# Kernel optimization log

Measured on AMD Instinct MI355X. Metric: run time of the kernel, lower is better.

Reference implementation:

```python
import jax, jax.numpy as jnp
import numpy as np

B, H, W, C, NC = 4, 64, 64, 64, 19


def setup_inputs() -> dict:
    key = jax.random.key(0)
    ks = jax.random.split(key, 12)
    s = 0.05  # small init so sigmoid scores are not saturated
    return {
        "feature": jax.random.normal(ks[0], (B, H, W, C), dtype=jnp.float32),
        "predict": jax.random.normal(ks[1], (B, H, W, NC), dtype=jnp.float32),
        # height attention params (dim = H); k_linear in source is unused (q reused as k)
        "hq_w": jax.random.normal(ks[2], (H, H), dtype=jnp.float32) * s,
        "hq_b": jnp.zeros((H,), dtype=jnp.float32),
        "hv_w": jax.random.normal(ks[3], (H, H), dtype=jnp.float32) * s,
        "hv_b": jnp.zeros((H,), dtype=jnp.float32),
        # width attention params (dim = W)
        "wq_w": jax.random.normal(ks[4], (W, W), dtype=jnp.float32) * s,
        "wq_b": jnp.zeros((W,), dtype=jnp.float32),
        "wv_w": jax.random.normal(ks[5], (W, W), dtype=jnp.float32) * s,
        "wv_b": jnp.zeros((W,), dtype=jnp.float32),
        # gating scalars (nn.Parameter(torch.zeros(1)) in source; random here to exercise path)
        "h_gate": jax.random.normal(ks[6], (1,), dtype=jnp.float32) * 0.5,
        "w_gate": jax.random.normal(ks[7], (1,), dtype=jnp.float32) * 0.5,
        # 1x1 conv num_classes -> 1 (stored as [NC, 1] matrix; 1x1 conv == per-pixel linear)
        "conv_w": jax.random.normal(ks[8], (NC, 1), dtype=jnp.float32) * s,
        "conv_b": jnp.zeros((1,), dtype=jnp.float32),
    }


def _self_atten(x, wq, bq, wv, bv, dim):
    # Source uses q_linear for BOTH q and k (k_linear dead), softmax replaced by sigmoid.
    q = x @ wq + bq                                   # [B, N, dim]
    v = x @ wv + bv                                   # [B, N, dim]
    scores = jax.nn.sigmoid(jnp.einsum('bnd,bmd->bnm', q, q) / jnp.sqrt(jnp.float32(dim)))
    return jnp.einsum('bnm,bmd->bnd', scores, v)      # [B, N, dim]


def _axial(x, hq_w, hq_b, hv_w, hv_b, wq_w, wq_b, wv_w, wv_b, h_gate, w_gate):
    b, h, w, c = x.shape
    # height attention: seq = W*C, feature dim = H
    xh = x.transpose(0, 2, 3, 1).reshape(b, w * c, h)
    xh = _self_atten(xh, hq_w, hq_b, hv_w, hv_b, h)
    xh = xh.reshape(b, w, c, h).transpose(0, 3, 1, 2)  # back to [B,H,W,C]
    x = xh * h_gate + x
    # width attention: seq = H*C, feature dim = W
    xw = x.transpose(0, 1, 3, 2).reshape(b, h * c, w)
    xw = _self_atten(xw, wq_w, wq_b, wv_w, wv_b, w)
    xw = xw.reshape(b, h, c, w).transpose(0, 1, 3, 2)  # back to [B,H,W,C]
    x = xw * w_gate + x
    return x


def reference(feature, predict, hq_w, hq_b, hv_w, hv_b, wq_w, wq_b, wv_w, wv_b,
              h_gate, w_gate, conv_w, conv_b):
    feat = feature + _axial(feature, hq_w, hq_b, hv_w, hv_b,
                            wq_w, wq_b, wv_w, wv_b, h_gate, w_gate)
    p = 1.0 - jax.nn.sigmoid(predict)                 # [B,H,W,NC]
    p = p @ conv_w + conv_b                           # 1x1 conv -> [B,H,W,1]
    return p * feat                                   # broadcast gate -> [B,H,W,C]
```

## Files before the change

kernel.cpp:

```cpp
#include <hip/hip_runtime.h>

typedef _Float16 f16x8 __attribute__((ext_vector_type(8)));
typedef __fp16   fp16x2 __attribute__((ext_vector_type(2)));
typedef float f32x16 __attribute__((ext_vector_type(16)));

__device__ __forceinline__ unsigned pkrtz(float a, float b) {
    fp16x2 h = __builtin_amdgcn_cvt_pkrtz(a, b);
    union { fp16x2 h; unsigned u; } c; c.h = h; return c.u;
}

__device__ __forceinline__ unsigned short f2h(float f) {
    _Float16 h = (_Float16)f;
    union { _Float16 h; unsigned short s; } c; c.h = h; return c.s;
}

__device__ __forceinline__ float sig_from_t(float t) {
    return __builtin_amdgcn_rcpf(1.0f + __builtin_exp2f(t));
}

__global__ __launch_bounds__(256) void prep_kernel(
    const float* __restrict__ src,
    const float* __restrict__ wq, const float* __restrict__ bq,
    const float* __restrict__ wv, const float* __restrict__ bv,
    unsigned short* __restrict__ Qg, unsigned short* __restrict__ Vtg)
{
    __shared__ float slab[64][65];
    __shared__ float wqs[4096];
    __shared__ float wvs[4096];

    const int t  = threadIdx.x;
    const int bx = blockIdx.x, b = blockIdx.y;

    {
        const float4* wq4 = (const float4*)wq;
        const float4* wv4 = (const float4*)wv;
        float4* q4 = (float4*)wqs; float4* v4 = (float4*)wvs;
        #pragma unroll
        for (int i = 0; i < 4; ++i) {
            q4[i*256 + t] = wq4[i*256 + t];
            v4[i*256 + t] = wv4[i*256 + t];
        }
    }
    {
        const int k = t >> 2, c0 = (t & 3) << 4;
        const size_t sb = (size_t)b*262144 + (size_t)k*4096 + (size_t)bx*64 + c0;
        #pragma unroll
        for (int i = 0; i < 4; ++i)
            *(float4*)&slab[k][c0 + i*4] = *(const float4*)&src[sb + i*4];
    }
    __syncthreads();

    const int c = t & 63, jg = t >> 6;
    float qa[16], va[16];
    #pragma unroll
    for (int jj = 0; jj < 16; ++jj) { qa[jj] = bq[jg*16+jj]; va[jj] = bv[jg*16+jj]; }
    for (int k = 0; k < 64; ++k) {
        const float xv = slab[k][c];
        const float* wqr = &wqs[k*64 + jg*16];
        const float* wvr = &wvs[k*64 + jg*16];
        #pragma unroll
        for (int jj = 0; jj < 16; ++jj) {
            qa[jj] += xv * wqr[jj];
            va[jj] += xv * wvr[jj];
        }
    }
    const int token = bx*64 + c;
    union { unsigned u[8]; uint4 v[2]; } qp;
    #pragma unroll
    for (int jj = 0; jj < 8; ++jj) qp.u[jj] = pkrtz(qa[2*jj], qa[2*jj+1]);
    const size_t qoff = ((size_t)b*4096 + token)*64 + jg*16;
    *(uint4*)&Qg[qoff]     = qp.v[0];
    *(uint4*)&Qg[qoff + 8] = qp.v[1];
    #pragma unroll
    for (int jj = 0; jj < 16; ++jj)
        Vtg[((size_t)b*64 + jg*16 + jj)*4096 + token] = f2h(va[jj]);
}

__global__ __launch_bounds__(256) void prep_w_kernel(
    const float* __restrict__ feature, const float* __restrict__ Pin,
    const float* __restrict__ gate,
    const float* __restrict__ wq, const float* __restrict__ bq,
    const float* __restrict__ wv, const float* __restrict__ bv,
    unsigned short* __restrict__ Qg, unsigned short* __restrict__ Vtg,
    float* __restrict__ x1out, int nsplit)
{
    __shared__ float slab[64][65];
    __shared__ float wqs[4096];
    __shared__ float wvs[4096];

    const int t  = threadIdx.x;
    const int bx = blockIdx.x, b = blockIdx.y;

    {
        const float4* wq4 = (const float4*)wq;
        const float4* wv4 = (const float4*)wv;
        float4* q4 = (float4*)wqs; float4* v4 = (float4*)wvs;
        #pragma unroll
        for (int i = 0; i < 4; ++i) {
            q4[i*256 + t] = wq4[i*256 + t];
            v4[i*256 + t] = wv4[i*256 + t];
        }
    }
    {
        const int k = t >> 2, c0 = (t & 3) << 4;
        const size_t off = (size_t)bx*4096 + (size_t)k*64 + c0;
        const size_t fb  = (size_t)b*262144 + off;
        const float g = gate[0];
        #pragma unroll
        for (int i = 0; i < 4; ++i) {
            float4 v  = *(const float4*)&feature[fb + i*4];
            float sx = 0.f, sy = 0.f, sz = 0.f, sw = 0.f;
            for (int ks = 0; ks < nsplit; ++ks) {
                float4 pk = *(const float4*)&Pin[((size_t)(ks*4 + b) << 18) + off + i*4];
                sx += pk.x; sy += pk.y; sz += pk.z; sw += pk.w;
            }
            v.x += g * sx; v.y += g * sy; v.z += g * sz; v.w += g * sw;
            *(float4*)&slab[k][c0 + i*4] = v;
            *(float4*)&x1out[fb + i*4] = v;
        }
    }
    __syncthreads();

    const int c = t & 63, jg = t >> 6;
    float qa[16], va[16];
    #pragma unroll
    for (int jj = 0; jj < 16; ++jj) { qa[jj] = bq[jg*16+jj]; va[jj] = bv[jg*16+jj]; }
    for (int k = 0; k < 64; ++k) {
        const float xv = slab[k][c];
        const float* wqr = &wqs[k*64 + jg*16];
        const float* wvr = &wvs[k*64 + jg*16];
        #pragma unroll
        for (int jj = 0; jj < 16; ++jj) {
            qa[jj] += xv * wqr[jj];
            va[jj] += xv * wvr[jj];
        }
    }
    const int token = bx*64 + c;
    union { unsigned u[8]; uint4 v[2]; } qp;
    #pragma unroll
    for (int jj = 0; jj < 8; ++jj) qp.u[jj] = pkrtz(qa[2*jj], qa[2*jj+1]);
    const size_t qoff = ((size_t)b*4096 + token)*64 + jg*16;
    *(uint4*)&Qg[qoff]     = qp.v[0];
    *(uint4*)&Qg[qoff + 8] = qp.v[1];
    #pragma unroll
    for (int jj = 0; jj < 16; ++jj)
        Vtg[((size_t)b*64 + jg*16 + jj)*4096 + token] = f2h(va[jj]);
}

__global__ __launch_bounds__(256) void attn_kernel(
    const unsigned short* __restrict__ Qg,
    const unsigned short* __restrict__ Vtg,
    float* __restrict__ P)
{
    __shared__ unsigned short Ksh[64][72];
    __shared__ unsigned short Vts[64][72];

    const int t = threadIdx.x;
    const int mb = blockIdx.x, b = blockIdx.y, ksplit = blockIdx.z;
    const int nsp = gridDim.z;
    const int niter = 64 / nsp;
    const int keybase = ksplit * (4096 / nsp);
    const int lane = t & 63, w = t >> 6;
    const int l32 = lane & 31, hi = lane >> 5;

    const unsigned short* Qbase = Qg  + (size_t)b*262144;
    const unsigned short* Vbase = Vtg + (size_t)b*262144;

    f16x8 qb[4];
    {
        const unsigned short* qrow = Qbase + (size_t)(mb*128 + w*32 + l32)*64 + hi*8;
        const _Float16 sc = (_Float16)(-0.180336880f);
        #pragma unroll
        for (int s = 0; s < 4; ++s) {
            f16x8 q = *(const f16x8*)(qrow + s*16);
            qb[s] = q * sc;
        }
    }

    f32x16 y[2];
    #pragma unroll
    for (int i = 0; i < 16; ++i) { y[0][i] = 0.f; y[1][i] = 0.f; }

    const int lrow = t >> 2;
    const int loff = (t & 3) << 4;
    {
        const uint4* gk = (const uint4*)(Qbase + (size_t)(keybase + lrow)*64 + loff);
        uint4 k0 = gk[0], k1 = gk[1];
        const uint4* gv = (const uint4*)(Vbase + (size_t)lrow*4096 + keybase + loff);
        uint4 v0 = gv[0], v1 = gv[1];
        *(uint4*)&Ksh[lrow][loff]     = k0;
        *(uint4*)&Ksh[lrow][loff + 8] = k1;
        *(uint4*)&Vts[lrow][loff]     = v0;
        *(uint4*)&Vts[lrow][loff + 8] = v1;
    }
    __syncthreads();

    for (int kb = 0; kb < niter; ++kb) {
        uint4 nk0 = {0,0,0,0}, nk1 = {0,0,0,0}, nv0 = {0,0,0,0}, nv1 = {0,0,0,0};
        if (kb < niter - 1) {
            const int keyn = keybase + (kb + 1)*64;
            const uint4* gk = (const uint4*)(Qbase + (size_t)(keyn + lrow)*64 + loff);
            nk0 = gk[0]; nk1 = gk[1];
            const uint4* gv = (const uint4*)(Vbase + (size_t)lrow*4096 + keyn + loff);
            nv0 = gv[0]; nv1 = gv[1];
        }

        f32x16 tt[2];
        #pragma unroll
        for (int i = 0; i < 16; ++i) { tt[0][i] = 0.f; tt[1][i] = 0.f; }
        #pragma unroll
        for (int s = 0; s < 4; ++s) {
            const int co = s*16 + hi*8;
            f16x8 ka0 = *(const f16x8*)&Ksh[l32][co];
            f16x8 ka1 = *(const f16x8*)&Ksh[32 + l32][co];
            tt[0] = __builtin_amdgcn_mfma_f32_32x32x16_f16(ka0, qb[s], tt[0], 0,0,0);
            tt[1] = __builtin_amdgcn_mfma_f32_32x32x16_f16(ka1, qb[s], tt[1], 0,0,0);
        }

        #pragma unroll
        for (int u = 0; u < 2; ++u) {
            float sg[16];
            #pragma unroll
            for (int r = 0; r < 16; ++r) sg[r] = sig_from_t(tt[u][r]);
            #pragma unroll
            for (int ksh = 0; ksh < 2; ++ksh) {
                const int bR = ksh*8;
                unsigned Pa = pkrtz(sg[bR+0], sg[bR+1]);
                unsigned Pb = pkrtz(sg[bR+2], sg[bR+3]);
                unsigned Qa = pkrtz(sg[bR+4], sg[bR+5]);
                unsigned Qb = pkrtz(sg[bR+6], sg[bR+7]);
                unsigned xPa = __shfl_xor(Pa, 32);
                unsigned xPb = __shfl_xor(Pb, 32);
                unsigned xQa = __shfl_xor(Qa, 32);
                unsigned xQb = __shfl_xor(Qb, 32);
                union { unsigned u[4]; f16x8 v; } sa;
                sa.u[0] = hi ? xQa : Pa;
                sa.u[1] = hi ? xQb : Pb;
                sa.u[2] = hi ? Qa : xPa;
                sa.u[3] = hi ? Qb : xPb;

                const int ks = u*2 + ksh;
                const int co = ks*16 + hi*8;
                f16x8 vb0 = *(const f16x8*)&Vts[l32][co];
                f16x8 vb1 = *(const f16x8*)&Vts[32 + l32][co];
                y[0] = __builtin_amdgcn_mfma_f32_32x32x16_f16(sa.v, vb0, y[0], 0,0,0);
                y[1] = __builtin_amdgcn_mfma_f32_32x32x16_f16(sa.v, vb1, y[1], 0,0,0);
            }
        }

        __syncthreads();
        if (kb < niter - 1) {
            *(uint4*)&Ksh[lrow][loff]     = nk0;
            *(uint4*)&Ksh[lrow][loff + 8] = nk1;
            *(uint4*)&Vts[lrow][loff]     = nv0;
            *(uint4*)&Vts[lrow][loff + 8] = nv1;
        }
        __syncthreads();
    }

    float* Pp = P + (((size_t)(ksplit*4 + b)) << 18);
    const int token0 = mb*128 + w*32 + hi*4;
    #pragma unroll
    for (int dt = 0; dt < 2; ++dt) {
        const int d = dt*32 + l32;
        #pragma unroll
        for (int g = 0; g < 4; ++g) {
            float4 v;
            v.x = y[dt][4*g+0]; v.y = y[dt][4*g+1];
            v.z = y[dt][4*g+2]; v.w = y[dt][4*g+3];
            *(float4*)&Pp[(size_t)d*4096 + token0 + 8*g] = v;
        }
    }
}

__global__ __launch_bounds__(256) void final_kernel(
    const float* __restrict__ feature, const float* __restrict__ x1,
    const float* __restrict__ Pin, const float* __restrict__ predict,
    const float* __restrict__ conv_w, const float* __restrict__ conv_b,
    const float* __restrict__ gate, float* __restrict__ out, int nsplit)
{
    const int i4 = blockIdx.x * 256 + threadIdx.x;
    const int j = i4 << 2;
    const int pix = j >> 6;
    const float* row = predict + (size_t)pix * 19;
    float pv = conv_b[0];
    #pragma unroll
    for (int i = 0; i < 19; ++i) {
        float sg = __builtin_amdgcn_rcpf(1.0f + __builtin_exp2f(-1.442695041f * row[i]));
        pv += (1.0f - sg) * conv_w[i];
    }

    const int b = j >> 18, h = (j >> 12) & 63, d = (j >> 6) & 63, c = j & 63;
    const size_t pif = ((size_t)(b*64 + d) << 12) + h*64 + c;
    float sx = 0.f, sy = 0.f, sz = 0.f, sw = 0.f;
    for (int ks = 0; ks < nsplit; ++ks) {
        float4 pk = *(const float4*)&Pin[((size_t)ks << 20) + pif];
        sx += pk.x; sy += pk.y; sz += pk.z; sw += pk.w;
    }
    const float g = gate[0];
    float4 f = ((const float4*)feature)[i4];
    float4 x = ((const float4*)x1)[i4];
    float4 o;
    o.x = pv * (f.x + x.x + g * sx);
    o.y = pv * (f.y + x.y + g * sy);
    o.z = pv * (f.z + x.z + g * sz);
    o.w = pv * (f.w + x.w + g * sw);
    ((float4*)out)[i4] = o;
}

extern "C" void kernel_launch(void* const* d_in, const int* in_sizes, int n_in,
                              void* d_out, int out_size, void* d_ws, size_t ws_size,
                              hipStream_t stream) {
    const float* feature = (const float*)d_in[0];
    const float* predict = (const float*)d_in[1];
    const float* hq_w = (const float*)d_in[2];
    const float* hq_b = (const float*)d_in[3];
    const float* hv_w = (const float*)d_in[4];
    const float* hv_b = (const float*)d_in[5];
    const float* wq_w = (const float*)d_in[6];
    const float* wq_b = (const float*)d_in[7];
    const float* wv_w = (const float*)d_in[8];
    const float* wv_b = (const float*)d_in[9];
    const float* h_gate = (const float*)d_in[10];
    const float* w_gate = (const float*)d_in[11];
    const float* conv_w = (const float*)d_in[12];
    const float* conv_b = (const float*)d_in[13];
    float* out = (float*)d_out;

    char* ws = (char*)d_ws;
    unsigned short* Qg  = (unsigned short*)(ws);
    unsigned short* Vtg = (unsigned short*)(ws + (2u << 20));
    float*          x1  = (float*)(ws + (4u << 20));
    float*          P   = (float*)(ws + (8u << 20));
    const int nsplit = 4;

    dim3 blk(256);
    prep_kernel<<<dim3(64, 4), blk, 0, stream>>>(feature, hq_w, hq_b, hv_w, hv_b,
                                                 Qg, Vtg);
    attn_kernel<<<dim3(32, 4, nsplit), blk, 0, stream>>>(Qg, Vtg, P);
    prep_w_kernel<<<dim3(64, 4), blk, 0, stream>>>(feature, P, h_gate,
                                                   wq_w, wq_b, wv_w, wv_b,
                                                   Qg, Vtg, x1, nsplit);
    attn_kernel<<<dim3(32, 4, nsplit), blk, 0, stream>>>(Qg, Vtg, P);
    final_kernel<<<dim3(1024), blk, 0, stream>>>(feature, x1, P, predict,
                                                 conv_w, conv_b, w_gate, out, nsplit);
}
```

Baseline: 189.2 us.

## Compute Q/V projections with fp16 MFMA using pre-transposed fp16 weights

Replaces the scalar FP32 LDS-based Q and V projection loops with 32x32x16 fp16 MFMA instructions. A new small kernel converts and transposes the four weight matrices to fp16 once per call. The two prep kernels are merged into one parameterized kernel with stride arguments, and the input tile is staged as fp16 in shared memory. This cuts per-block LDS weight loading and FMA work, but adds a launch, rounds inputs and weights to fp16, and switches to scalar uncoalesced stores for Q and the feature loads.

```diff
diff --git a/kernel.cpp b/kernel.cpp
--- a/kernel.cpp
+++ b/kernel.cpp
@@ -18,133 +18,108 @@
     return __builtin_amdgcn_rcpf(1.0f + __builtin_exp2f(t));
 }
 
+__global__ __launch_bounds__(256) void wprep_kernel(
+    const float* __restrict__ w0, const float* __restrict__ w1,
+    const float* __restrict__ w2, const float* __restrict__ w3,
+    unsigned short* __restrict__ Wt)
+{
+    __shared__ float m[64][65];
+    const float* src = (blockIdx.x == 0) ? w0 : (blockIdx.x == 1) ? w1
+                     : (blockIdx.x == 2) ? w2 : w3;
+    const int t = threadIdx.x;
+    const int k = t >> 2, c0 = (t & 3) << 4;
+    #pragma unroll
+    for (int i = 0; i < 4; ++i)
+        *(float4*)&m[k][c0 + i*4] = *(const float4*)&src[k*64 + c0 + i*4];
+    __syncthreads();
+    const int j = t >> 2, k0 = (t & 3) << 4;
+    union { unsigned u[8]; uint4 v[2]; } o;
+    #pragma unroll
+    for (int p = 0; p < 8; ++p) o.u[p] = pkrtz(m[k0 + 2*p][j], m[k0 + 2*p + 1][j]);
+    unsigned short* dst = Wt + blockIdx.x*4096 + j*64 + k0;
+    *(uint4*)dst       = o.v[0];
+    *(uint4*)(dst + 8) = o.v[1];
+}
+
 __global__ __launch_bounds__(256) void prep_kernel(
-    const float* __restrict__ src,
-    const float* __restrict__ wq, const float* __restrict__ bq,
-    const float* __restrict__ wv, const float* __restrict__ bv,
-    unsigned short* __restrict__ Qg, unsigned short* __restrict__ Vtg)
+    const float* __restrict__ src, const float* __restrict__ Pin,
+    const float* __restrict__ gate,
+    const unsigned short* __restrict__ Wqt, const unsigned short* __restrict__ Wvt,
+    const float* __restrict__ bq, const float* __restrict__ bv,
+    unsigned short* __restrict__ Qg, unsigned short* __restrict__ Vtg,
+    float* __restrict__ x1out, int sK, int sF, int nsplit)
 {
-    __shared__ float slab[64][65];
-    __shared__ float wqs[4096];
-    __shared__ float wvs[4096];
-
-    const int t  = threadIdx.x;
+    __shared__ unsigned short Xt[64][76];
+
+    const int t = threadIdx.x;
     const int bx = blockIdx.x, b = blockIdx.y;
 
     {
-        const float4* wq4 = (const float4*)wq;
-        const float4* wv4 = (const float4*)wv;
-        float4* q4 = (float4*)wqs; float4* v4 = (float4*)wvs;
-        #pragma unroll
-        for (int i = 0; i < 4; ++i) {
-            q4[i*256 + t] = wq4[i*256 + t];
-            v4[i*256 + t] = wv4[i*256 + t];
-        }
-    }
+        const int c = t & 63, kq = t >> 6;
+        const float g = Pin ? gate[0] : 0.f;
+        float vals[16];
+        #pragma unroll
+        for (int kk = 0; kk < 16; ++kk) {
+            const int k = kq*16 + kk;
+            const size_t off = (size_t)k*sK + (size_t)bx*sF + c;
+            float v = src[(size_t)b*262144 + off];
+            if (Pin) {
+                float s = 0.f;
+                for (int ks = 0; ks < nsplit; ++ks)
+                    s += Pin[((size_t)(ks*4 + b) << 18) + off];
+                v += g * s;
+                x1out[(size_t)b*262144 + off] = v;
+            }
+            vals[kk] = v;
+        }
+        union { unsigned u[8]; uint4 q[2]; } pk;
+        #pragma unroll
+        for (int p = 0; p < 8; ++p) pk.u[p] = pkrtz(vals[2*p], vals[2*p+1]);
+        *(uint4*)&Xt[c][kq*16]     = pk.q[0];
+        *(uint4*)&Xt[c][kq*16 + 8] = pk.q[1];
+    }
+    __syncthreads();
+
+    const int lane = t & 63, w = t >> 6;
+    const int l32 = lane & 31, hi = lane >> 5;
+    const int tt = w & 1, jt = w >> 1;
+
+    f16x8 xf[4], wqf[4], wvf[4];
+    #pragma unroll
+    for (int s = 0; s < 4; ++s)
+        xf[s] = *(const f16x8*)&Xt[tt*32 + l32][s*16 + hi*8];
     {
-        const int k = t >> 2, c0 = (t & 3) << 4;
-        const size_t sb = (size_t)b*262144 + (size_t)k*4096 + (size_t)bx*64 + c0;
-        #pragma unroll
-        for (int i = 0; i < 4; ++i)
-            *(float4*)&slab[k][c0 + i*4] = *(const float4*)&src[sb + i*4];
-    }
-    __syncthreads();
-
-    const int c = t & 63, jg = t >> 6;
-    float qa[16], va[16];
-    #pragma unroll
-    for (int jj = 0; jj < 16; ++jj) { qa[jj] = bq[jg*16+jj]; va[jj] = bv[jg*16+jj]; }
-    for (int k = 0; k < 64; ++k) {
-        const float xv = slab[k][c];
-        const float* wqr = &wqs[k*64 + jg*16];
-        const float* wvr = &wvs[k*64 + jg*16];
-        #pragma unroll
-        for (int jj = 0; jj < 16; ++jj) {
-            qa[jj] += xv * wqr[jj];
-            va[jj] += xv * wvr[jj];
-        }
-    }
-    const int token = bx*64 + c;
-    union { unsigned u[8]; uint4 v[2]; } qp;
-    #pragma unroll
-    for (int jj = 0; jj < 8; ++jj) qp.u[jj] = pkrtz(qa[2*jj], qa[2*jj+1]);
-    const size_t qoff = ((size_t)b*4096 + token)*64 + jg*16;
-    *(uint4*)&Qg[qoff]     = qp.v[0];
-    *(uint4*)&Qg[qoff + 8] = qp.v[1];
-    #pragma unroll
-    for (int jj = 0; jj < 16; ++jj)
-        Vtg[((size_t)b*64 + jg*16 + jj)*4096 + token] = f2h(va[jj]);
-}
-
-__global__ __launch_bounds__(256) void prep_w_kernel(
-    const float* __restrict__ feature, const float* __restrict__ Pin,
-    const float* __restrict__ gate,
-    const float* __restrict__ wq, const float* __restrict__ bq,
-    const float* __restrict__ wv, const float* __restrict__ bv,
-    unsigned short* __restrict__ Qg, unsigned short* __restrict__ Vtg,
-    float* __restrict__ x1out, int nsplit)
-{
-    __shared__ float slab[64][65];
-    __shared__ float wqs[4096];
-    __shared__ float wvs[4096];
-
-    const int t  = threadIdx.x;
-    const int bx = blockIdx.x, b = blockIdx.y;
-
-    {
-        const float4* wq4 = (const float4*)wq;
-        const float4* wv4 = (const float4*)wv;
-        float4* q4 = (float4*)wqs; float4* v4 = (float4*)wvs;
-        #pragma unroll
-        for (int i = 0; i < 4; ++i) {
-            q4[i*256 + t] = wq4[i*256 + t];
-            v4[i*256 + t] = wv4[i*256 + t];
-        }
-    }
-    {
-        const int k = t >> 2, c0 = (t & 3) << 4;
-        const size_t off = (size_t)bx*4096 + (size_t)k*64 + c0;
-        const size_t fb  = (size_t)b*262144 + off;
-        const float g = gate[0];
-        #pragma unroll
-        for (int i = 0; i < 4; ++i) {
-            float4 v  = *(const float4*)&feature[fb + i*4];
-            float sx = 0.f, sy = 0.f, sz = 0.f, sw = 0.f;
-            for (int ks = 0; ks < nsplit; ++ks) {
-                float4 pk = *(const float4*)&Pin[((size_t)(ks*4 + b) << 18) + off + i*4];
-                sx += pk.x; sy += pk.y; sz += pk.z; sw += pk.w;
-            }
-            v.x += g * sx; v.y += g * sy; v.z += g * sz; v.w += g * sw;
-            *(float4*)&slab[k][c0 + i*4] = v;
-            *(float4*)&x1out[fb + i*4] = v;
-        }
-    }
-    __syncthreads();
-
-    const int c = t & 63, jg = t >> 6;
-    float qa[16], va[16];
-    #pragma unroll
-    for (int jj = 0; jj < 16; ++jj) { qa[jj] = bq[jg*16+jj]; va[jj] = bv[jg*16+jj]; }
-    for (int k = 0; k < 64; ++k) {
-        const float xv = slab[k][c];
-        const float* wqr = &wqs[k*64 + jg*16];
-        const float* wvr = &wvs[k*64 + jg*16];
-        #pragma unroll
-        for (int jj = 0; jj < 16; ++jj) {
-            qa[jj] += xv * wqr[jj];
-            va[jj] += xv * wvr[jj];
-        }
-    }
-    const int token = bx*64 + c;
-    union { unsigned u[8]; uint4 v[2]; } qp;
-    #pragma unroll
-    for (int jj = 0; jj < 8; ++jj) qp.u[jj] = pkrtz(qa[2*jj], qa[2*jj+1]);
-    const size_t qoff = ((size_t)b*4096 + token)*64 + jg*16;
-    *(uint4*)&Qg[qoff]     = qp.v[0];
-    *(uint4*)&Qg[qoff + 8] = qp.v[1];
-    #pragma unroll
-    for (int jj = 0; jj < 16; ++jj)
-        Vtg[((size_t)b*64 + jg*16 + jj)*4096 + token] = f2h(va[jj]);
+        const unsigned short* qr = Wqt + (size_t)(jt*32 + l32)*64 + hi*8;
+        const unsigned short* vr = Wvt + (size_t)(jt*32 + l32)*64 + hi*8;
+        #pragma unroll
+        for (int s = 0; s < 4; ++s) {
+            wqf[s] = *(const f16x8*)(qr + s*16);
+            wvf[s] = *(const f16x8*)(vr + s*16);
+        }
+    }
+
+    f32x16 qa, va;
+    #pragma unroll
+    for (int i = 0; i < 16; ++i) { qa[i] = 0.f; va[i] = 0.f; }
+    #pragma unroll
+    for (int s = 0; s < 4; ++s) {
+        qa = __builtin_amdgcn_mfma_f32_32x32x16_f16(xf[s], wqf[s], qa, 0,0,0);
+        va = __builtin_amdgcn_mfma_f32_32x32x16_f16(wvf[s], xf[s], va, 0,0,0);
+    }
+
+    const float bqv = bq[jt*32 + l32];
+    const size_t qbase = (size_t)b*4096 + bx*64;
+    #pragma unroll
+    for (int r = 0; r < 16; ++r) {
+        const int c = tt*32 + (r & 3) + 8*(r >> 2) + 4*hi;
+        Qg[(qbase + c)*64 + jt*32 + l32] = f2h(qa[r] + bqv);
+    }
+    const int ctok = bx*64 + tt*32 + l32;
+    #pragma unroll
+    for (int r = 0; r < 16; ++r) {
+        const int j = jt*32 + (r & 3) + 8*(r >> 2) + 4*hi;
+        Vtg[(size_t)b*262144 + (size_t)j*4096 + ctok] = f2h(va[r] + bv[j]);
+    }
 }
 
 __global__ __launch_bounds__(256) void attn_kernel(
@@ -332,15 +307,18 @@
     unsigned short* Vtg = (unsigned short*)(ws + (2u << 20));
     float*          x1  = (float*)(ws + (4u << 20));
     float*          P   = (float*)(ws + (8u << 20));
+    unsigned short* Wt  = (unsigned short*)(ws + (24u << 20));
     const int nsplit = 4;
 
     dim3 blk(256);
-    prep_kernel<<<dim3(64, 4), blk, 0, stream>>>(feature, hq_w, hq_b, hv_w, hv_b,
-                                                 Qg, Vtg);
+    wprep_kernel<<<dim3(4), blk, 0, stream>>>(hq_w, hv_w, wq_w, wv_w, Wt);
+    prep_kernel<<<dim3(64, 4), blk, 0, stream>>>(feature, nullptr, nullptr,
+                                                 Wt, Wt + 4096, hq_b, hv_b,
+                                                 Qg, Vtg, nullptr, 4096, 64, 0);
     attn_kernel<<<dim3(32, 4, nsplit), blk, 0, stream>>>(Qg, Vtg, P);
-    prep_w_kernel<<<dim3(64, 4), blk, 0, stream>>>(feature, P, h_gate,
-                                                   wq_w, wq_b, wv_w, wv_b,
-                                                   Qg, Vtg, x1, nsplit);
+    prep_kernel<<<dim3(64, 4), blk, 0, stream>>>(feature, P, h_gate,
+                                                 Wt + 8192, Wt + 12288, wq_b, wv_b,
+                                                 Qg, Vtg, x1, 64, 4096, nsplit);
     attn_kernel<<<dim3(32, 4, nsplit), blk, 0, stream>>>(Qg, Vtg, P);
     final_kernel<<<dim3(1024), blk, 0, stream>>>(feature, x1, P, predict,
                                                  conv_w, conv_b, w_gate, out, nsplit);
```

New measurement: 197.5 us. +4.4%, slower.

## Double-buffer K/V LDS tiles, drop cross-lane shuffles via permuted V layout

Applied to the files above, without the earlier changes.

Splits the K and V shared-memory tiles into two buffers so the next tile is written into the spare buffer while the current one is read, which removes one of the two barriers per iteration. It also drops the 32-lane shuffle exchange of sigmoid scores by permuting the V tile columns at store time so each lane's own MFMA output lines up with the B operand. Finally, it computes two sigmoids with one reciprocal, clamping the exponent to avoid overflow. The costs are double the LDS footprint, which can lower occupancy, and slightly different rounding in the paired-reciprocal sigmoid.

```diff
diff --git a/kernel.cpp b/kernel.cpp
--- a/kernel.cpp
+++ b/kernel.cpp
@@ -12,10 +12,6 @@
 __device__ __forceinline__ unsigned short f2h(float f) {
     _Float16 h = (_Float16)f;
     union { _Float16 h; unsigned short s; } c; c.h = h; return c.s;
-}
-
-__device__ __forceinline__ float sig_from_t(float t) {
-    return __builtin_amdgcn_rcpf(1.0f + __builtin_exp2f(t));
 }
 
 __global__ __launch_bounds__(256) void prep_kernel(
@@ -152,8 +148,8 @@
     const unsigned short* __restrict__ Vtg,
     float* __restrict__ P)
 {
-    __shared__ unsigned short Ksh[64][72];
-    __shared__ unsigned short Vts[64][72];
+    __shared__ unsigned short Ksh[2][64][72];
+    __shared__ unsigned short Vts[2][64][72];
 
     const int t = threadIdx.x;
     const int mb = blockIdx.x, b = blockIdx.y, ksplit = blockIdx.z;
@@ -188,14 +184,18 @@
         uint4 k0 = gk[0], k1 = gk[1];
         const uint4* gv = (const uint4*)(Vbase + (size_t)lrow*4096 + keybase + loff);
         uint4 v0 = gv[0], v1 = gv[1];
-        *(uint4*)&Ksh[lrow][loff]     = k0;
-        *(uint4*)&Ksh[lrow][loff + 8] = k1;
-        *(uint4*)&Vts[lrow][loff]     = v0;
-        *(uint4*)&Vts[lrow][loff + 8] = v1;
+        *(uint4*)&Ksh[0][lrow][loff]     = k0;
+        *(uint4*)&Ksh[0][lrow][loff + 8] = k1;
+        uint4 pa = { v0.x, v0.y, v1.x, v1.y };
+        uint4 pb = { v0.z, v0.w, v1.z, v1.w };
+        *(uint4*)&Vts[0][lrow][loff]     = pa;
+        *(uint4*)&Vts[0][lrow][loff + 8] = pb;
     }
     __syncthreads();
 
     for (int kb = 0; kb < niter; ++kb) {
+        const int cur = kb & 1, nxt = cur ^ 1;
+
         uint4 nk0 = {0,0,0,0}, nk1 = {0,0,0,0}, nv0 = {0,0,0,0}, nv1 = {0,0,0,0};
         if (kb < niter - 1) {
             const int keyn = keybase + (kb + 1)*64;
@@ -211,49 +211,48 @@
         #pragma unroll
         for (int s = 0; s < 4; ++s) {
             const int co = s*16 + hi*8;
-            f16x8 ka0 = *(const f16x8*)&Ksh[l32][co];
-            f16x8 ka1 = *(const f16x8*)&Ksh[32 + l32][co];
+            f16x8 ka0 = *(const f16x8*)&Ksh[cur][l32][co];
+            f16x8 ka1 = *(const f16x8*)&Ksh[cur][32 + l32][co];
             tt[0] = __builtin_amdgcn_mfma_f32_32x32x16_f16(ka0, qb[s], tt[0], 0,0,0);
             tt[1] = __builtin_amdgcn_mfma_f32_32x32x16_f16(ka1, qb[s], tt[1], 0,0,0);
         }
 
         #pragma unroll
         for (int u = 0; u < 2; ++u) {
-            float sg[16];
+            unsigned pk_[8];
             #pragma unroll
-            for (int r = 0; r < 16; ++r) sg[r] = sig_from_t(tt[u][r]);
+            for (int pr = 0; pr < 8; ++pr) {
+                float t0 = __builtin_fminf(tt[u][2*pr+0], 60.0f);
+                float t1 = __builtin_fminf(tt[u][2*pr+1], 60.0f);
+                float e0 = __builtin_exp2f(t0);
+                float e1 = __builtin_exp2f(t1);
+                float d0 = 1.0f + e0, d1 = 1.0f + e1;
+                float rr = __builtin_amdgcn_rcpf(d0 * d1);
+                pk_[pr] = pkrtz(rr * d1, rr * d0);
+            }
             #pragma unroll
-            for (int ksh = 0; ksh < 2; ++ksh) {
-                const int bR = ksh*8;
-                unsigned Pa = pkrtz(sg[bR+0], sg[bR+1]);
-                unsigned Pb = pkrtz(sg[bR+2], sg[bR+3]);
-                unsigned Qa = pkrtz(sg[bR+4], sg[bR+5]);
-                unsigned Qb = pkrtz(sg[bR+6], sg[bR+7]);
-                unsigned xPa = __shfl_xor(Pa, 32);
-                unsigned xPb = __shfl_xor(Pb, 32);
-                unsigned xQa = __shfl_xor(Qa, 32);
-                unsigned xQb = __shfl_xor(Qb, 32);
-                union { unsigned u[4]; f16x8 v; } sa;
-                sa.u[0] = hi ? xQa : Pa;
-                sa.u[1] = hi ? xQb : Pb;
-                sa.u[2] = hi ? Qa : xPa;
-                sa.u[3] = hi ? Qb : xPb;
-
-                const int ks = u*2 + ksh;
+            for (int sp = 0; sp < 2; ++sp) {
+                union { unsigned u4[4]; f16x8 v; } sa;
+                sa.u4[0] = pk_[sp*4 + 0];
+                sa.u4[1] = pk_[sp*4 + 1];
+                sa.u4[2] = pk_[sp*4 + 2];
+                sa.u4[3] = pk_[sp*4 + 3];
+                const int ks = u*2 + sp;
                 const int co = ks*16 + hi*8;
-                f16x8 vb0 = *(const f16x8*)&Vts[l32][co];
-                f16x8 vb1 = *(const f16x8*)&Vts[32 + l32][co];
+                f16x8 vb0 = *(const f16x8*)&Vts[cur][l32][co];
+                f16x8 vb1 = *(const f16x8*)&Vts[cur][32 + l32][co];
                 y[0] = __builtin_amdgcn_mfma_f32_32x32x16_f16(sa.v, vb0, y[0], 0,0,0);
                 y[1] = __builtin_amdgcn_mfma_f32_32x32x16_f16(sa.v, vb1, y[1], 0,0,0);
             }
         }
 
-        __syncthreads();
         if (kb < niter - 1) {
-            *(uint4*)&Ksh[lrow][loff]     = nk0;
-            *(uint4*)&Ksh[lrow][loff + 8] = nk1;
-            *(uint4*)&Vts[lrow][loff]     = nv0;
-            *(uint4*)&Vts[lrow][loff + 8] = nv1;
+            *(uint4*)&Ksh[nxt][lrow][loff]     = nk0;
+            *(uint4*)&Ksh[nxt][lrow][loff + 8] = nk1;
+            uint4 pa = { nv0.x, nv0.y, nv1.x, nv1.y };
+            uint4 pb = { nv0.z, nv0.w, nv1.z, nv1.w };
+            *(uint4*)&Vts[nxt][lrow][loff]     = pa;
+            *(uint4*)&Vts[nxt][lrow][loff + 8] = pb;
         }
         __syncthreads();
     }
```

After: 188.8 us. No clear change (-0.2%).
